# Kernel tuning notes

Measured on AMD Instinct MI355X. Metric: run time of the kernel, lower is better.

## Reference

```python
import jax, jax.numpy as jnp
import numpy as np

B, D, M = 256, 8, 6  # batch, path dimension, signature depth


def setup_inputs() -> dict:
    key = jax.random.key(0)
    k1, k2 = jax.random.split(key)
    siglen = sum(D ** k for k in range(1, M + 1))  # 299592
    x = jax.random.normal(k1, (B, siglen), dtype=jnp.float32)
    # scales kept positive-ish and away from 0, like realistic path scalings
    y = jax.random.uniform(k2, (B, D), dtype=jnp.float32) + 0.5
    return {"x": x, "y": y, "m": M}


def reference(x, y, m):
    """iisignature.sigscale: level-k signature term S_{i1..ik} -> S_{i1..ik} * prod_j y[i_j].

    x: [B, siglen] flattened signature, levels 1..m concatenated, each level k
       stored as d^k entries in row-major (lexicographic word) order.
    y: [B, d] per-sample per-coordinate scale.
    """
    b, d = y.shape
    outs = []
    off = 0
    f = y  # level-1 scale factors, [B, d^1]
    for k in range(1, m + 1):
        n = d ** k
        outs.append(x[:, off:off + n] * f)
        off += n
        if k < m:
            # extend word factors: f[(i1..ik, j)] = f[(i1..ik)] * y[j]
            f = (f[:, :, None] * y[:, None, :]).reshape(b, d ** (k + 1))
    return jnp.concatenate(outs, axis=1)
```

## Files before the change

kernel.cpp:

```cpp
#include <hip/hip_runtime.h>


#define SIGLEN 299592
#define NQ     74898

typedef float f4 __attribute__((ext_vector_type(4)));

__device__ __forceinline__ float quad_g(int q,
                                        const float* __restrict__ f1,
                                        const float* __restrict__ f2,
                                        const float* __restrict__ f3,
                                        int& nout) {
    const int pos = q << 2;
    int n; float g;
    if (pos >= 37448) {
        n = pos - 37448; const int p = n >> 3; g = f3[p >> 6] * f2[p & 63];
    } else if (pos >= 4680) {
        n = pos - 4680;  const int p = n >> 3; g = f3[p >> 3] * f1[p & 7];
    } else if (pos >= 584) {
        n = pos - 584;   g = f3[n >> 3];
    } else if (pos >= 72) {
        n = pos - 72;    g = f2[n >> 3];
    } else if (pos >= 8) {
        n = pos - 8;     g = f1[n >> 3];
    } else {
        n = pos;         g = 1.0f;
    }
    nout = n;
    return g;
}

__global__ __launch_bounds__(256) void sigscale_kernel(
    const float* __restrict__ x,
    const float* __restrict__ y,
    float* __restrict__ out)
{
    __shared__ __align__(16) float f1[8];
    __shared__ float f2[64];
    __shared__ float f3[512];

    const int b   = blockIdx.y;
    const int tid = threadIdx.x;

    if (tid < 8) f1[tid] = y[b * 8 + tid];
    __syncthreads();
    if (tid < 64) f2[tid] = f1[tid >> 3] * f1[tid & 7];
    __syncthreads();
    for (int i = tid; i < 512; i += 256) f3[i] = f2[i >> 3] * f1[i & 7];
    __syncthreads();

    const f4 ylo = *reinterpret_cast<const f4*>(&f1[0]);
    const f4 yhi = *reinterpret_cast<const f4*>(&f1[4]);

    const f4* __restrict__ xr   = reinterpret_cast<const f4*>(x + (size_t)b * SIGLEN);
    f4* __restrict__       orow = reinterpret_cast<f4*>(out + (size_t)b * SIGLEN);

    const int s = (-(b << 1)) & 7;

    if (blockIdx.x == 0 && tid < s) {
        const int q = tid;
        int n; const float g = quad_g(q, f1, f2, f3, n);
        const f4 yl = (n & 4) ? yhi : ylo;
        orow[q] = xr[q] * g * yl;
    }

    constexpr int STRIDE = 2048;
    int q = s + blockIdx.x * 256 + tid;

    for (; q < NQ - 7 * STRIDE; q += 8 * STRIDE) {
        f4 v[8]; float g[8]; int n[8];
        #pragma unroll
        for (int j = 0; j < 8; ++j) v[j] = xr[q + j * STRIDE];
        #pragma unroll
        for (int j = 0; j < 8; ++j) g[j] = quad_g(q + j * STRIDE, f1, f2, f3, n[j]);
        #pragma unroll
        for (int j = 0; j < 8; ++j) {
            const f4 a = (n[j] & 4) ? yhi : ylo;
            orow[q + j * STRIDE] = v[j] * (g[j] * a);
        }
    }

    for (; q < NQ; q += STRIDE) {
        int n; const float g = quad_g(q, f1, f2, f3, n);
        const f4 yl = (n & 4) ? yhi : ylo;
        orow[q] = xr[q] * (g * yl);
    }
}

extern "C" void kernel_launch(void* const* d_in, const int* in_sizes, int n_in,
                              void* d_out, int out_size, void* d_ws, size_t ws_size,
                              hipStream_t stream) {
    const float* x = (const float*)d_in[0];
    const float* y = (const float*)d_in[1];
    float* out = (float*)d_out;

    dim3 grid(8, 256);
    sigscale_kernel<<<grid, 256, 0, stream>>>(x, y, out);
}
```

Measured before the change: 130.9 us.

## Software-pipeline row loads with nontemporal accesses and smaller batches

The main loop now handles batches of 4 strided quads and prefetches the next batch into registers while the current one is computed and stored, instead of loading 8 and then storing 8. All global loads and stores use nontemporal builtins to avoid polluting caches on this pure streaming kernel. The launch bounds now request 8 blocks per CU so register use is capped. Together these aim to keep more memory requests in flight per wave. The double-buffered registers and occupancy hint could instead cause spills or leave fewer loads outstanding per wave.

```diff
diff --git a/kernel.cpp b/kernel.cpp
--- a/kernel.cpp
+++ b/kernel.cpp
@@ -30,7 +30,7 @@
     return g;
 }
 
-__global__ __launch_bounds__(256) void sigscale_kernel(
+__global__ __launch_bounds__(256, 8) void sigscale_kernel(
     const float* __restrict__ x,
     const float* __restrict__ y,
     float* __restrict__ out)
@@ -61,29 +61,50 @@
         const int q = tid;
         int n; const float g = quad_g(q, f1, f2, f3, n);
         const f4 yl = (n & 4) ? yhi : ylo;
-        orow[q] = xr[q] * g * yl;
+        orow[q] = xr[q] * (g * yl);
     }
 
     constexpr int STRIDE = 2048;
+    constexpr int BATCH  = 4;
+    constexpr int SPAN   = BATCH * STRIDE;
+
     int q = s + blockIdx.x * 256 + tid;
 
-    for (; q < NQ - 7 * STRIDE; q += 8 * STRIDE) {
-        f4 v[8]; float g[8]; int n[8];
+    f4 v[BATCH];
+    bool have = (q + (BATCH - 1) * STRIDE) < NQ;
+    if (have) {
         #pragma unroll
-        for (int j = 0; j < 8; ++j) v[j] = xr[q + j * STRIDE];
+        for (int j = 0; j < BATCH; ++j)
+            v[j] = __builtin_nontemporal_load(&xr[q + j * STRIDE]);
+    }
+    while (have) {
+        const int qn = q + SPAN;
+        const bool have_next = (qn + (BATCH - 1) * STRIDE) < NQ;
+        f4 w[BATCH];
+        if (have_next) {
+            #pragma unroll
+            for (int j = 0; j < BATCH; ++j)
+                w[j] = __builtin_nontemporal_load(&xr[qn + j * STRIDE]);
+        }
         #pragma unroll
-        for (int j = 0; j < 8; ++j) g[j] = quad_g(q + j * STRIDE, f1, f2, f3, n[j]);
-        #pragma unroll
-        for (int j = 0; j < 8; ++j) {
-            const f4 a = (n[j] & 4) ? yhi : ylo;
-            orow[q + j * STRIDE] = v[j] * (g[j] * a);
+        for (int j = 0; j < BATCH; ++j) {
+            int n; const float g = quad_g(q + j * STRIDE, f1, f2, f3, n);
+            const f4 a = (n & 4) ? yhi : ylo;
+            __builtin_nontemporal_store(v[j] * (g * a), &orow[q + j * STRIDE]);
         }
+        if (have_next) {
+            #pragma unroll
+            for (int j = 0; j < BATCH; ++j) v[j] = w[j];
+        }
+        q = qn;
+        have = have_next;
     }
 
     for (; q < NQ; q += STRIDE) {
         int n; const float g = quad_g(q, f1, f2, f3, n);
         const f4 yl = (n & 4) ? yhi : ylo;
-        orow[q] = xr[q] * (g * yl);
+        const f4 t = __builtin_nontemporal_load(&xr[q]);
+        __builtin_nontemporal_store(t * (g * yl), &orow[q]);
     }
 }
 
```

Result: faster. 123.9 us (-5.3%).
